# Optimization experiments

Measured on AMD Instinct MI355X. Metric: run time of the kernel, lower is better.

Reference implementation:

```python
import jax, jax.numpy as jnp
import numpy as np

N, E, D_IN, D_HID, D_OUT = 50000, 800000, 128, 128, 64

def setup_inputs() -> dict:
    key = jax.random.key(0)
    ks = jax.random.split(key, 20)
    inp = {
        'x': jax.random.normal(ks[0], (N, D_IN), dtype=jnp.float32),
        'edge_index': jax.random.randint(ks[1], (2, E), 0, N, dtype=jnp.int64),
        'edge_attr': jax.random.normal(ks[2], (E, 16), dtype=jnp.float32),
        'edge_weight': jax.random.uniform(ks[3], (E,), dtype=jnp.float32),
    }
    dims = [(D_IN, D_HID), (D_HID, D_HID), (D_HID, D_OUT)]
    for i, (di, do) in enumerate(dims):
        s = 1.0 / np.sqrt(di)
        inp[f'Wl{i}'] = jax.random.uniform(ks[4 + 5 * i], (di, do), minval=-s, maxval=s, dtype=jnp.float32)
        inp[f'bl{i}'] = jnp.zeros((do,), dtype=jnp.float32)
        inp[f'Wr{i}'] = jax.random.uniform(ks[5 + 5 * i], (di, do), minval=-s, maxval=s, dtype=jnp.float32)
        inp[f'Ws{i}'] = jax.random.uniform(ks[6 + 5 * i], (di, do), minval=-s, maxval=s, dtype=jnp.float32)
        inp[f'bs{i}'] = jnp.zeros((do,), dtype=jnp.float32)
    return inp


def _sage(x, src, dst, Wl, bl, Wr):
    # mean aggregation of source features at target nodes (PyG SAGEConv)
    msg = x[src]                                               # [E, d] gather
    ssum = jax.ops.segment_sum(msg, dst, num_segments=N)        # [N, d]
    cnt = jax.ops.segment_sum(jnp.ones((src.shape[0],), x.dtype), dst, num_segments=N)
    agg = ssum / jnp.maximum(cnt, 1.0)[:, None]
    return agg @ Wl + bl + x @ Wr                               # lin_l(agg) + lin_r(x)


def reference(x, edge_index, edge_attr, edge_weight,
              Wl0, bl0, Wr0, Ws0, bs0,
              Wl1, bl1, Wr1, Ws1, bs1,
              Wl2, bl2, Wr2, Ws2, bs2):
    src, dst = edge_index[0], edge_index[1]
    h = jax.nn.relu(_sage(x, src, dst, Wl0, bl0, Wr0) + x @ Ws0 + bs0)
    h = jax.nn.relu(_sage(h, src, dst, Wl1, bl1, Wr1) + h @ Ws1 + bs1)
    out = _sage(h, src, dst, Wl2, bl2, Wr2) + h @ Ws2 + bs2
    return out
```

## Files before the change

kernel.cpp:

```cpp
#include <hip/hip_runtime.h>
#include <hip/hip_bf16.h>


#define LB __launch_bounds__

typedef __attribute__((ext_vector_type(8))) short short8;
typedef __attribute__((ext_vector_type(4))) float f32x4;

__device__ __forceinline__ unsigned short bf16_rne(float f) {
  unsigned u = __builtin_bit_cast(unsigned, f);
  unsigned r = u + 0x7fffu + ((u >> 16) & 1u);
  return (unsigned short)(r >> 16);
}
__device__ __forceinline__ float bf16_to_f(unsigned short us) {
  return __builtin_bit_cast(float, (unsigned)us << 16);
}
__device__ __forceinline__ float bits_to_f(unsigned u) {
  return __builtin_bit_cast(float, u);
}

__device__ __forceinline__ void async16(const void* g, void* l) {
  __builtin_amdgcn_global_load_lds((const __attribute__((address_space(1))) unsigned*)g,
                                   (__attribute__((address_space(3))) unsigned*)l, 16, 0, 0);
}

#define BCAP 8192
#define P1_CHUNK 4096

__device__ __forceinline__ void p1_body(int bid, const int* __restrict__ src,
                                        const int* __restrict__ dst, int* __restrict__ bcnt,
                                        int2* __restrict__ pairs, int E) {
  __shared__ int cnt[256];
  __shared__ int base[256];
  const int tid = threadIdx.x;
  cnt[tid] = 0;
  __syncthreads();
  const int e0 = bid * P1_CHUNK;
  int myb[16], myr[16], mys[16], myd[16];
#pragma unroll
  for (int i = 0; i < 16; ++i) {
    int e = e0 + i * 256 + tid;
    myb[i] = -1;
    if (e < E) {
      int s = src[e], d = dst[e];
      int b = d >> 8;
      myb[i] = b;
      mys[i] = s;
      myd[i] = d;
      myr[i] = atomicAdd(&cnt[b], 1);
    }
  }
  __syncthreads();
  base[tid] = (cnt[tid] > 0) ? atomicAdd(&bcnt[tid], cnt[tid]) : 0;
  __syncthreads();
#pragma unroll
  for (int i = 0; i < 16; ++i) {
    int b = myb[i];
    if (b >= 0) {
      int p = base[b] + myr[i];
      if (p < BCAP) pairs[(size_t)b * BCAP + p] = make_int2(mys[i], myd[i]);
    }
  }
}

__device__ __forceinline__ void p234_body(int b, const int2* __restrict__ pairs,
                                          const int* __restrict__ bcnt, int* __restrict__ gcounter,
                                          int* __restrict__ row_start, int* __restrict__ deg_arr,
                                          float* __restrict__ scale, int* __restrict__ srcs, int N) {
  __shared__ int h[256];
  __shared__ int sc[256];
  __shared__ int cur[256];
  __shared__ int shared_bb;
  const int tid = threadIdx.x;
  h[tid] = 0;
  __syncthreads();
  int m = bcnt[b];
  if (m > BCAP) m = BCAP;
  for (int i = tid; i < m; i += 256) {
    atomicAdd(&h[pairs[(size_t)b * BCAP + i].y & 255], 1);
  }
  __syncthreads();
  const int deg = h[tid];
  sc[tid] = deg;
  __syncthreads();
  for (int off = 1; off < 256; off <<= 1) {
    int add = (tid >= off) ? sc[tid - off] : 0;
    __syncthreads();
    sc[tid] += add;
    __syncthreads();
  }
  if (tid == 0) shared_bb = atomicAdd(gcounter, sc[255]);
  __syncthreads();
  const int abs_off = shared_bb + sc[tid] - deg;
  const int node = b * 256 + tid;
  if (node < N) {
    row_start[node] = abs_off;
    deg_arr[node] = deg;
    scale[node] = 1.0f / (float)(deg > 1 ? deg : 1);
  }
  cur[tid] = abs_off;
  __syncthreads();
  for (int i = tid; i < m; i += 256) {
    int2 pr = pairs[(size_t)b * BCAP + i];
    int p = atomicAdd(&cur[pr.y & 255], 1);
    srcs[p] = pr.x;
  }
}

__device__ __forceinline__ void wpack_body(int wb, const float* __restrict__ Wl0,
                                           const float* __restrict__ Wr0,
                                           const float* __restrict__ Ws0,
                                           const float* __restrict__ bl0,
                                           const float* __restrict__ bs0,
                                           const float* __restrict__ Wl1,
                                           const float* __restrict__ Wr1,
                                           const float* __restrict__ Ws1,
                                           const float* __restrict__ bl1,
                                           const float* __restrict__ bs1,
                                           const float* __restrict__ Wl2,
                                           const float* __restrict__ Wr2,
                                           const float* __restrict__ Ws2,
                                           const float* __restrict__ bl2,
                                           const float* __restrict__ bs2, ushort* __restrict__ Bh0,
                                           ushort* __restrict__ Bo0, float* __restrict__ bb0,
                                           ushort* __restrict__ Bh1, ushort* __restrict__ Bo1,
                                           float* __restrict__ bb1, ushort* __restrict__ Bh2,
                                           ushort* __restrict__ Bo2, float* __restrict__ bb2) {
  const int layer = wb >> 7;
  const int xb = wb & 127;
  const float *Wl, *Wr, *Ws, *bl, *bs;
  ushort *Bh, *Bo;
  float* bb;
  int M;
  if (layer == 0) {
    Wl = Wl0; Wr = Wr0; Ws = Ws0; bl = bl0; bs = bs0; Bh = Bh0; Bo = Bo0; bb = bb0; M = 256;
  } else if (layer == 1) {
    Wl = Wl1; Wr = Wr1; Ws = Ws1; bl = bl1; bs = bs1; Bh = Bh1; Bo = Bo1; bb = bb1; M = 256;
  } else {
    Wl = Wl2; Wr = Wr2; Ws = Ws2; bl = bl2; bs = bs2; Bh = Bh2; Bo = Bo2; bb = bb2; M = 128;
  }
  const int DO = M / 2;
  int idx = xb * 256 + (int)threadIdx.x;
  if (idx < 128 * M) {
    int k = idx / M, c = idx - k * M;
    float v = (c < DO) ? Wl[k * DO + c] : (Wr[k * DO + (c - DO)] + Ws[k * DO + (c - DO)]);
    unsigned short h = bf16_rne(v);
    unsigned short l = bf16_rne(v - bf16_to_f(h));
    int d = ((k >> 3) * M + c) * 8 + (k & 7);
    Bh[d] = h;
    Bo[d] = l;
  }
  if (idx < DO) bb[idx] = bl[idx] + bs[idx];
}

__device__ __forceinline__ void split8v(f32x4 f0, f32x4 f1, short8& h, short8& l) {
  float f[8] = {f0[0], f0[1], f0[2], f0[3], f1[0], f1[1], f1[2], f1[3]};
#pragma unroll
  for (int j = 0; j < 8; ++j) {
    unsigned u = __builtin_bit_cast(unsigned, f[j]);
    h[j] = (short)(u >> 16);
    l[j] = (short)bf16_rne(f[j] - bits_to_f(u & 0xffff0000u));
  }
}

template <int M, bool AFP32>
__device__ __forceinline__ void gemm_body(int bx, const float* __restrict__ Af,
                                          const ushort* __restrict__ Ahi,
                                          const ushort* __restrict__ Alo,
                                          const ushort* __restrict__ Bhi,
                                          const ushort* __restrict__ Blo, ushort* __restrict__ Yb,
                                          float* __restrict__ Z, int n, char* smem) {
  constexpr int DO = M / 2;
  constexpr int NWC = (M >= 256) ? 4 : 2;
  constexpr int NWR = 4 / NWC;
  constexpr int BROWS = 32 * NWR;
  const int tid = threadIdx.x;
  const int w = tid >> 6, l = tid & 63;
  const int q = l >> 4, m16 = l & 15;
  const int blockRow0 = bx * BROWS;
  const int rowBase = blockRow0 + (w / NWC) * 32;
  const int colBase = (w % NWC) * 64;
  const int wbase = tid & ~63;

  if (AFP32) {
#pragma unroll
    for (int r = 0; r < BROWS / 8; ++r) {
      int ell = r * 256 + tid;
      int row = ell >> 5, gl = ell & 31;
      int grow = blockRow0 + row;
      if (grow >= n) grow = n - 1;
      int gs = gl ^ (row & 15);
      async16(Af + (size_t)grow * 128 + gs * 4, smem + (size_t)(r * 256 + wbase) * 16);
    }
  } else {
#pragma unroll
    for (int r = 0; r < BROWS / 16; ++r) {
      int ell = r * 256 + tid;
      int row = ell >> 4, gl = ell & 15;
      int grow = blockRow0 + row;
      if (grow >= n) grow = n - 1;
      int gs = gl ^ (row & 15);
      async16(Ahi + (size_t)grow * 128 + gs * 8, smem + (size_t)(r * 256 + wbase) * 16);
      async16(Alo + (size_t)grow * 128 + gs * 8,
              smem + (size_t)BROWS * 256 + (size_t)(r * 256 + wbase) * 16);
    }
  }
  __syncthreads();

  f32x4 acc[2][4] = {};
  const int rl0 = (w / NWC) * 32 + m16;

#pragma unroll
  for (int s = 0; s < 4; ++s) {
    short8 ah[2], al[2], bh[4], bo[4];
#pragma unroll
    for (int i = 0; i < 2; ++i) {
      int rl = rl0 + i * 16;
      if (AFP32) {
        int g0 = (2 * (s * 4 + q)) ^ m16;
        int g1 = (2 * (s * 4 + q) + 1) ^ m16;
        f32x4 fa = *(const f32x4*)(smem + (size_t)rl * 512 + g0 * 16);
        f32x4 fb = *(const f32x4*)(smem + (size_t)rl * 512 + g1 * 16);
        split8v(fa, fb, ah[i], al[i]);
      } else {
        int g = (s * 4 + q) ^ m16;
        ah[i] = *(const short8*)(smem + (size_t)rl * 256 + g * 16);
        al[i] = *(const short8*)(smem + (size_t)BROWS * 256 + (size_t)rl * 256 + g * 16);
      }
    }
    const int kb = s * 4 + q;
#pragma unroll
    for (int j = 0; j < 4; ++j) {
      size_t off = ((size_t)kb * M + colBase + j * 16 + m16) * 8;
      bh[j] = *(const short8*)(Bhi + off);
      bo[j] = *(const short8*)(Blo + off);
    }
#pragma unroll
    for (int i = 0; i < 2; ++i)
#pragma unroll
      for (int j = 0; j < 4; ++j) {
        acc[i][j] = __builtin_amdgcn_mfma_f32_16x16x32_bf16(ah[i], bh[j], acc[i][j], 0, 0, 0);
        acc[i][j] = __builtin_amdgcn_mfma_f32_16x16x32_bf16(ah[i], bo[j], acc[i][j], 0, 0, 0);
        acc[i][j] = __builtin_amdgcn_mfma_f32_16x16x32_bf16(al[i], bh[j], acc[i][j], 0, 0, 0);
      }
  }

#pragma unroll
  for (int i = 0; i < 2; ++i) {
    int rb = rowBase + i * 16 + q * 4;
#pragma unroll
    for (int j = 0; j < 4; ++j) {
      int c = colBase + j * 16 + m16;
#pragma unroll
      for (int r = 0; r < 4; ++r) {
        int row = rb + r;
        if (row < n) {
          float v = acc[i][j][r];
          if (c < DO)
            Yb[(size_t)row * DO + c] = bf16_rne(v);
          else
            Z[(size_t)row * DO + (c - DO)] = v;
        }
      }
    }
  }
}

template <int M, bool AFP32>
__global__ LB(256, 3) void mfma_gemm_kernel(const float* __restrict__ Af,
                                            const ushort* __restrict__ Ahi,
                                            const ushort* __restrict__ Alo,
                                            const ushort* __restrict__ Bhi,
                                            const ushort* __restrict__ Blo,
                                            ushort* __restrict__ Yb, float* __restrict__ Z, int n) {
  constexpr int LDSB = AFP32 ? (32 * 512) : ((M >= 256 ? 32 : 64) * 512);
  __shared__ __align__(16) char smem[LDSB];
  gemm_body<M, AFP32>(blockIdx.x, Af, Ahi, Alo, Bhi, Blo, Yb, Z, n, smem);
}

__global__ LB(256) void fused_wpack_p1(const int* __restrict__ src, const int* __restrict__ dst,
                                       int* __restrict__ bcnt, int2* __restrict__ pairs, int E,
                                       int NP1, const float* Wl0, const float* Wr0, const float* Ws0,
                                       const float* bl0, const float* bs0, const float* Wl1,
                                       const float* Wr1, const float* Ws1, const float* bl1,
                                       const float* bs1, const float* Wl2, const float* Wr2,
                                       const float* Ws2, const float* bl2, const float* bs2,
                                       ushort* Bh0, ushort* Bo0, float* bb0, ushort* Bh1,
                                       ushort* Bo1, float* bb1, ushort* Bh2, ushort* Bo2,
                                       float* bb2) {
  if ((int)blockIdx.x < NP1) {
    p1_body(blockIdx.x, src, dst, bcnt, pairs, E);
  } else {
    wpack_body(blockIdx.x - NP1, Wl0, Wr0, Ws0, bl0, bs0, Wl1, Wr1, Ws1, bl1, bs1, Wl2, Wr2, Ws2,
               bl2, bs2, Bh0, Bo0, bb0, Bh1, Bo1, bb1, Bh2, Bo2, bb2);
  }
}

__global__ LB(256, 3) void fused_p234_gemm0(const int2* __restrict__ pairs,
                                            const int* __restrict__ bcnt, int* __restrict__ gcounter,
                                            int* __restrict__ row_start, int* __restrict__ deg_arr,
                                            float* __restrict__ scale, int* __restrict__ srcs, int N,
                                            const float* __restrict__ x,
                                            const ushort* __restrict__ Bh0,
                                            const ushort* __restrict__ Bo0, ushort* __restrict__ Yb,
                                            float* __restrict__ Zf, int NB) {
  __shared__ __align__(16) char smem[32 * 512];
  if ((int)blockIdx.x < NB) {
    p234_body(blockIdx.x, pairs, bcnt, gcounter, row_start, deg_arr, scale, srcs, N);
  } else {
    gemm_body<256, true>(blockIdx.x - NB, x, nullptr, nullptr, Bh0, Bo0, Yb, Zf, N, smem);
  }
}

__global__ LB(256) void agg128_kernel(const ushort* __restrict__ Y, const float* __restrict__ Z,
                                      const int* __restrict__ row_start,
                                      const int* __restrict__ deg_arr, const int* __restrict__ srcs,
                                      const float* __restrict__ scale,
                                      const float* __restrict__ bsum, unsigned* __restrict__ Hhi,
                                      unsigned* __restrict__ Hlo, int n) {
  int node = blockIdx.x * 4 + (threadIdx.x >> 6);
  if (node >= n) return;
  const int lane = threadIdx.x & 63;
  const int li = lane & 31;
  const int half = lane >> 5;
  const int e0 = row_start[node];
  const int cnt = deg_arr[node];
  const int end = e0 + cnt;
  const int c1 = cnt < 64 ? cnt : 64;
  int idx = (lane < c1) ? srcs[e0 + lane] : 0;
  const uint2* Yu = (const uint2*)Y;
  float a0 = 0.f, a1 = 0.f, a2 = 0.f, a3 = 0.f;

  int j = 0;
  for (; j + 16 <= c1; j += 16) {
    int s[8];
#pragma unroll
    for (int t = 0; t < 8; ++t) s[t] = __shfl(idx, j + 2 * t + half);
    uint2 u[8];
#pragma unroll
    for (int t = 0; t < 8; ++t) u[t] = Yu[(size_t)s[t] * 32 + li];
#pragma unroll
    for (int t = 0; t < 8; ++t) {
      a0 += bits_to_f(u[t].x << 16);
      a1 += bits_to_f(u[t].x & 0xffff0000u);
      a2 += bits_to_f(u[t].y << 16);
      a3 += bits_to_f(u[t].y & 0xffff0000u);
    }
  }
  if (j + 8 <= c1) {
    int s[4];
#pragma unroll
    for (int t = 0; t < 4; ++t) s[t] = __shfl(idx, j + 2 * t + half);
    uint2 u[4];
#pragma unroll
    for (int t = 0; t < 4; ++t) u[t] = Yu[(size_t)s[t] * 32 + li];
#pragma unroll
    for (int t = 0; t < 4; ++t) {
      a0 += bits_to_f(u[t].x << 16);
      a1 += bits_to_f(u[t].x & 0xffff0000u);
      a2 += bits_to_f(u[t].y << 16);
      a3 += bits_to_f(u[t].y & 0xffff0000u);
    }
    j += 8;
  }
  for (; j + 2 <= c1; j += 2) {
    int s = __shfl(idx, j + half);
    uint2 u = Yu[(size_t)s * 32 + li];
    a0 += bits_to_f(u.x << 16);
    a1 += bits_to_f(u.x & 0xffff0000u);
    a2 += bits_to_f(u.y << 16);
    a3 += bits_to_f(u.y & 0xffff0000u);
  }
  if (j < c1) {
    int s = __shfl(idx, j);
    if (half == 0) {
      uint2 u = Yu[(size_t)s * 32 + li];
      a0 += bits_to_f(u.x << 16);
      a1 += bits_to_f(u.x & 0xffff0000u);
      a2 += bits_to_f(u.y << 16);
      a3 += bits_to_f(u.y & 0xffff0000u);
    }
  }
  if (cnt > 64) {
    int e = e0 + 64;
    for (; e + 2 <= end; e += 2) {
      int s = srcs[e + half];
      uint2 u = Yu[(size_t)s * 32 + li];
      a0 += bits_to_f(u.x << 16);
      a1 += bits_to_f(u.x & 0xffff0000u);
      a2 += bits_to_f(u.y << 16);
      a3 += bits_to_f(u.y & 0xffff0000u);
    }
    if (e < end && half == 0) {
      int s = srcs[e];
      uint2 u = Yu[(size_t)s * 32 + li];
      a0 += bits_to_f(u.x << 16);
      a1 += bits_to_f(u.x & 0xffff0000u);
      a2 += bits_to_f(u.y << 16);
      a3 += bits_to_f(u.y & 0xffff0000u);
    }
  }
  a0 += __shfl(a0, lane ^ 32);
  a1 += __shfl(a1, lane ^ 32);
  a2 += __shfl(a2, lane ^ 32);
  a3 += __shfl(a3, lane ^ 32);

  float sc = scale[node];
  float4 z = ((const float4*)Z)[(size_t)node * 32 + li];
  float4 b = ((const float4*)bsum)[li];
  float o0 = fmaxf(z.x + sc * a0 + b.x, 0.f);
  float o1 = fmaxf(z.y + sc * a1 + b.y, 0.f);
  float o2 = fmaxf(z.z + sc * a2 + b.z, 0.f);
  float o3 = fmaxf(z.w + sc * a3 + b.w, 0.f);
  unsigned short h0 = bf16_rne(o0), h1 = bf16_rne(o1), h2 = bf16_rne(o2), h3 = bf16_rne(o3);
  if (half == 0) {
    uint2 hp;
    hp.x = (unsigned)h0 | ((unsigned)h1 << 16);
    hp.y = (unsigned)h2 | ((unsigned)h3 << 16);
    ((uint2*)Hhi)[(size_t)node * 32 + li] = hp;
  } else {
    unsigned short l0 = bf16_rne(o0 - bf16_to_f(h0));
    unsigned short l1 = bf16_rne(o1 - bf16_to_f(h1));
    unsigned short l2 = bf16_rne(o2 - bf16_to_f(h2));
    unsigned short l3 = bf16_rne(o3 - bf16_to_f(h3));
    uint2 lp;
    lp.x = (unsigned)l0 | ((unsigned)l1 << 16);
    lp.y = (unsigned)l2 | ((unsigned)l3 << 16);
    ((uint2*)Hlo)[(size_t)node * 32 + li] = lp;
  }
}

__global__ LB(256) void agg64_kernel(const ushort* __restrict__ Y, const float* __restrict__ Z,
                                     const int* __restrict__ row_start,
                                     const int* __restrict__ deg_arr, const int* __restrict__ srcs,
                                     const float* __restrict__ scale, const float* __restrict__ bsum,
                                     float* __restrict__ out, int n) {
  int node = blockIdx.x * 4 + (threadIdx.x >> 6);
  if (node >= n) return;
  const int lane = threadIdx.x & 63;
  const int li = lane & 15;
  const int qt = lane >> 4;
  const int e0 = row_start[node];
  const int cnt = deg_arr[node];
  const int end = e0 + cnt;
  const int c1 = cnt < 64 ? cnt : 64;
  int idx = (lane < c1) ? srcs[e0 + lane] : 0;
  const uint2* Yu = (const uint2*)Y;
  float a0 = 0.f, a1 = 0.f, a2 = 0.f, a3 = 0.f;

  int j = 0;
  for (; j + 16 <= c1; j += 16) {
    int s0 = __shfl(idx, j + qt);
    int s1 = __shfl(idx, j + 4 + qt);
    int s2 = __shfl(idx, j + 8 + qt);
    int s3 = __shfl(idx, j + 12 + qt);
    uint2 u0 = Yu[(size_t)s0 * 16 + li];
    uint2 u1 = Yu[(size_t)s1 * 16 + li];
    uint2 u2 = Yu[(size_t)s2 * 16 + li];
    uint2 u3 = Yu[(size_t)s3 * 16 + li];
    a0 += bits_to_f(u0.x << 16) + bits_to_f(u1.x << 16) + bits_to_f(u2.x << 16) +
          bits_to_f(u3.x << 16);
    a1 += bits_to_f(u0.x & 0xffff0000u) + bits_to_f(u1.x & 0xffff0000u) +
          bits_to_f(u2.x & 0xffff0000u) + bits_to_f(u3.x & 0xffff0000u);
    a2 += bits_to_f(u0.y << 16) + bits_to_f(u1.y << 16) + bits_to_f(u2.y << 16) +
          bits_to_f(u3.y << 16);
    a3 += bits_to_f(u0.y & 0xffff0000u) + bits_to_f(u1.y & 0xffff0000u) +
          bits_to_f(u2.y & 0xffff0000u) + bits_to_f(u3.y & 0xffff0000u);
  }
  for (; j + 4 <= c1; j += 4) {
    int s = __shfl(idx, j + qt);
    uint2 u = Yu[(size_t)s * 16 + li];
    a0 += bits_to_f(u.x << 16);
    a1 += bits_to_f(u.x & 0xffff0000u);
    a2 += bits_to_f(u.y << 16);
    a3 += bits_to_f(u.y & 0xffff0000u);
  }
  {
    int rem = c1 - j;
    if (rem > 0) {
      int s = __shfl(idx, j + (qt < rem ? qt : 0));
      if (qt < rem) {
        uint2 u = Yu[(size_t)s * 16 + li];
        a0 += bits_to_f(u.x << 16);
        a1 += bits_to_f(u.x & 0xffff0000u);
        a2 += bits_to_f(u.y << 16);
        a3 += bits_to_f(u.y & 0xffff0000u);
      }
    }
  }
  if (cnt > 64) {
    int e = e0 + 64;
    for (; e + 4 <= end; e += 4) {
      int s = srcs[e + qt];
      uint2 u = Yu[(size_t)s * 16 + li];
      a0 += bits_to_f(u.x << 16);
      a1 += bits_to_f(u.x & 0xffff0000u);
      a2 += bits_to_f(u.y << 16);
      a3 += bits_to_f(u.y & 0xffff0000u);
    }
    int rem = end - e;
    if (qt < rem) {
      int s = srcs[e + qt];
      uint2 u = Yu[(size_t)s * 16 + li];
      a0 += bits_to_f(u.x << 16);
      a1 += bits_to_f(u.x & 0xffff0000u);
      a2 += bits_to_f(u.y << 16);
      a3 += bits_to_f(u.y & 0xffff0000u);
    }
  }
  a0 += __shfl(a0, lane ^ 16);
  a1 += __shfl(a1, lane ^ 16);
  a2 += __shfl(a2, lane ^ 16);
  a3 += __shfl(a3, lane ^ 16);
  a0 += __shfl(a0, lane ^ 32);
  a1 += __shfl(a1, lane ^ 32);
  a2 += __shfl(a2, lane ^ 32);
  a3 += __shfl(a3, lane ^ 32);

  if (qt == 0) {
    float sc = scale[node];
    float4 z = ((const float4*)Z)[(size_t)node * 16 + li];
    float4 b = ((const float4*)bsum)[li];
    float4 o;
    o.x = z.x + sc * a0 + b.x;
    o.y = z.y + sc * a1 + b.y;
    o.z = z.z + sc * a2 + b.z;
    o.w = z.w + sc * a3 + b.w;
    ((float4*)out)[(size_t)node * 16 + li] = o;
  }
}

extern "C" void kernel_launch(void* const* d_in, const int* in_sizes, int n_in,
                              void* d_out, int out_size, void* d_ws, size_t ws_size,
                              hipStream_t stream) {
  const float* x = (const float*)d_in[0];
  const int* ei = (const int*)d_in[1];
  const int N = in_sizes[0] / 128;
  const int E = in_sizes[3];
  const int* src = ei;
  const int* dst = ei + E;
  const float* Wl[3] = {(const float*)d_in[4], (const float*)d_in[9], (const float*)d_in[14]};
  const float* bl[3] = {(const float*)d_in[5], (const float*)d_in[10], (const float*)d_in[15]};
  const float* Wr[3] = {(const float*)d_in[6], (const float*)d_in[11], (const float*)d_in[16]};
  const float* Ws[3] = {(const float*)d_in[7], (const float*)d_in[12], (const float*)d_in[17]};
  const float* bs[3] = {(const float*)d_in[8], (const float*)d_in[13], (const float*)d_in[18]};

  const int NB = (N + 255) >> 8;
  const int NP1 = (E + P1_CHUNK - 1) / P1_CHUNK;

  size_t off = 0;
  auto carve = [&](size_t bytes) -> char* {
    char* p = (char*)d_ws + off;
    off += (bytes + 255) & ~(size_t)255;
    return p;
  };
  int* row_start = (int*)carve((size_t)N * 4);
  int* deg_arr = (int*)carve((size_t)N * 4);
  int* bcnt = (int*)carve((size_t)NB * 4);
  int* gcounter = (int*)carve(256);
  float* scale = (float*)carve((size_t)N * 4);
  int* srcs = (int*)carve((size_t)E * 4);
  int2* pairs = (int2*)carve((size_t)NB * BCAP * 8);
  ushort* Hhi = (ushort*)carve((size_t)N * 128 * 2);
  ushort* Hlo = (ushort*)carve((size_t)N * 128 * 2);
  ushort* Yb = (ushort*)carve((size_t)N * 128 * 2);
  float* Zf = (float*)carve((size_t)N * 128 * 4);
  ushort* Bh[3];
  ushort* Bo[3];
  float* bsum[3];
  for (int i = 0; i < 3; ++i) {
    Bh[i] = (ushort*)carve(128 * 256 * 2);
    Bo[i] = (ushort*)carve(128 * 256 * 2);
    bsum[i] = (float*)carve(128 * 4);
  }
  (void)ws_size;
  (void)n_in;
  (void)out_size;

  size_t bcnt_pad = ((size_t)NB * 4 + 255) & ~(size_t)255;
  hipMemsetAsync(bcnt, 0, bcnt_pad + 4, stream);

  fused_wpack_p1<<<NP1 + 384, 256, 0, stream>>>(
      src, dst, bcnt, pairs, E, NP1, Wl[0], Wr[0], Ws[0], bl[0], bs[0], Wl[1], Wr[1], Ws[1], bl[1],
      bs[1], Wl[2], Wr[2], Ws[2], bl[2], bs[2], Bh[0], Bo[0], bsum[0], Bh[1], Bo[1], bsum[1], Bh[2],
      Bo[2], bsum[2]);

  int g32 = (N + 31) / 32;
  int g64 = (N + 63) / 64;
  int gAgg = (N + 3) / 4;

  fused_p234_gemm0<<<NB + g32, 256, 0, stream>>>(pairs, bcnt, gcounter, row_start, deg_arr, scale,
                                                 srcs, N, x, Bh[0], Bo[0], Yb, Zf, NB);
  agg128_kernel<<<gAgg, 256, 0, stream>>>(Yb, Zf, row_start, deg_arr, srcs, scale, bsum[0],
                                          (unsigned*)Hhi, (unsigned*)Hlo, N);
  mfma_gemm_kernel<256, false><<<g32, 256, 0, stream>>>(nullptr, Hhi, Hlo, Bh[1], Bo[1], Yb, Zf, N);
  agg128_kernel<<<gAgg, 256, 0, stream>>>(Yb, Zf, row_start, deg_arr, srcs, scale, bsum[1],
                                          (unsigned*)Hhi, (unsigned*)Hlo, N);
  mfma_gemm_kernel<128, false><<<g64, 256, 0, stream>>>(nullptr, Hhi, Hlo, Bh[2], Bo[2], Yb, Zf, N);
  agg64_kernel<<<gAgg, 256, 0, stream>>>(Yb, Zf, row_start, deg_arr, srcs, scale, bsum[2],
                                         (float*)d_out, N);
}
```

Baseline: 301.9 us.

## Fuse mean-aggregation into following layer's MFMA GEMM via LDS staging

```diff
diff --git a/kernel.cpp b/kernel.cpp
--- a/kernel.cpp
+++ b/kernel.cpp
@@ -163,13 +163,12 @@
   }
 }
 
-template <int M, bool AFP32>
-__device__ __forceinline__ void gemm_body(int bx, const float* __restrict__ Af,
-                                          const ushort* __restrict__ Ahi,
-                                          const ushort* __restrict__ Alo,
-                                          const ushort* __restrict__ Bhi,
-                                          const ushort* __restrict__ Blo, ushort* __restrict__ Yb,
-                                          float* __restrict__ Z, int n, char* smem) {
+template <int M>
+__device__ __forceinline__ void gemm_compute(int bx, const char* smem,
+                                             const ushort* __restrict__ Bhi,
+                                             const ushort* __restrict__ Blo,
+                                             ushort* __restrict__ Yb, float* __restrict__ Z,
+                                             int n) {
   constexpr int DO = M / 2;
   constexpr int NWC = (M >= 256) ? 4 : 2;
   constexpr int NWR = 4 / NWC;
@@ -177,35 +176,8 @@
   const int tid = threadIdx.x;
   const int w = tid >> 6, l = tid & 63;
   const int q = l >> 4, m16 = l & 15;
-  const int blockRow0 = bx * BROWS;
-  const int rowBase = blockRow0 + (w / NWC) * 32;
+  const int rowBase = bx * BROWS + (w / NWC) * 32;
   const int colBase = (w % NWC) * 64;
-  const int wbase = tid & ~63;
-
-  if (AFP32) {
-#pragma unroll
-    for (int r = 0; r < BROWS / 8; ++r) {
-      int ell = r * 256 + tid;
-      int row = ell >> 5, gl = ell & 31;
-      int grow = blockRow0 + row;
-      if (grow >= n) grow = n - 1;
-      int gs = gl ^ (row & 15);
-      async16(Af + (size_t)grow * 128 + gs * 4, smem + (size_t)(r * 256 + wbase) * 16);
-    }
-  } else {
-#pragma unroll
-    for (int r = 0; r < BROWS / 16; ++r) {
-      int ell = r * 256 + tid;
-      int row = ell >> 4, gl = ell & 15;
-      int grow = blockRow0 + row;
-      if (grow >= n) grow = n - 1;
-      int gs = gl ^ (row & 15);
-      async16(Ahi + (size_t)grow * 128 + gs * 8, smem + (size_t)(r * 256 + wbase) * 16);
-      async16(Alo + (size_t)grow * 128 + gs * 8,
-              smem + (size_t)BROWS * 256 + (size_t)(r * 256 + wbase) * 16);
-    }
-  }
-  __syncthreads();
 
   f32x4 acc[2][4] = {};
   const int rl0 = (w / NWC) * 32 + m16;
@@ -213,22 +185,16 @@
 #pragma unroll
   for (int s = 0; s < 4; ++s) {
     short8 ah[2], al[2], bh[4], bo[4];
+    const int kb = s * 4 + q;
 #pragma unroll
     for (int i = 0; i < 2; ++i) {
       int rl = rl0 + i * 16;
-      if (AFP32) {
-        int g0 = (2 * (s * 4 + q)) ^ m16;
-        int g1 = (2 * (s * 4 + q) + 1) ^ m16;
-        f32x4 fa = *(const f32x4*)(smem + (size_t)rl * 512 + g0 * 16);
-        f32x4 fb = *(const f32x4*)(smem + (size_t)rl * 512 + g1 * 16);
-        split8v(fa, fb, ah[i], al[i]);
-      } else {
-        int g = (s * 4 + q) ^ m16;
-        ah[i] = *(const short8*)(smem + (size_t)rl * 256 + g * 16);
-        al[i] = *(const short8*)(smem + (size_t)BROWS * 256 + (size_t)rl * 256 + g * 16);
-      }
-    }
-    const int kb = s * 4 + q;
+      int g0 = (2 * kb) ^ m16;
+      int g1 = (2 * kb + 1) ^ m16;
+      f32x4 fa = *(const f32x4*)(smem + (size_t)rl * 512 + g0 * 16);
+      f32x4 fb = *(const f32x4*)(smem + (size_t)rl * 512 + g1 * 16);
+      split8v(fa, fb, ah[i], al[i]);
+    }
 #pragma unroll
     for (int j = 0; j < 4; ++j) {
       size_t off = ((size_t)kb * M + colBase + j * 16 + m16) * 8;
@@ -266,16 +232,153 @@
   }
 }
 
-template <int M, bool AFP32>
-__global__ LB(256, 3) void mfma_gemm_kernel(const float* __restrict__ Af,
-                                            const ushort* __restrict__ Ahi,
-                                            const ushort* __restrict__ Alo,
-                                            const ushort* __restrict__ Bhi,
-                                            const ushort* __restrict__ Blo,
-                                            ushort* __restrict__ Yb, float* __restrict__ Z, int n) {
-  constexpr int LDSB = AFP32 ? (32 * 512) : ((M >= 256 ? 32 : 64) * 512);
-  __shared__ __align__(16) char smem[LDSB];
-  gemm_body<M, AFP32>(blockIdx.x, Af, Ahi, Alo, Bhi, Blo, Yb, Z, n, smem);
+__device__ __forceinline__ void gemm0_body(int bx, const float* __restrict__ x,
+                                           const ushort* __restrict__ Bh,
+                                           const ushort* __restrict__ Bo, ushort* __restrict__ Yb,
+                                           float* __restrict__ Z, int n, char* smem) {
+  const int tid = threadIdx.x;
+  const int wbase = tid & ~63;
+#pragma unroll
+  for (int r = 0; r < 4; ++r) {
+    int ell = r * 256 + tid;
+    int row = ell >> 5, gl = ell & 31;
+    int grow = bx * 32 + row;
+    if (grow >= n) grow = n - 1;
+    int gs = gl ^ (row & 15);
+    async16(x + (size_t)grow * 128 + gs * 4, smem + (size_t)(r * 256 + wbase) * 16);
+  }
+  __syncthreads();
+  gemm_compute<256>(bx, smem, Bh, Bo, Yb, Z, n);
+}
+
+__device__ __forceinline__ void agg_gather128(const uint2* __restrict__ Yu,
+                                              const int* __restrict__ srcs, int e0, int cnt,
+                                              int lane, int li, int half, float& a0, float& a1,
+                                              float& a2, float& a3) {
+  const int end = e0 + cnt;
+  const int c1 = cnt < 64 ? cnt : 64;
+  int idx = (lane < c1) ? srcs[e0 + lane] : 0;
+  int j = 0;
+  for (; j + 16 <= c1; j += 16) {
+    int s[8];
+#pragma unroll
+    for (int t = 0; t < 8; ++t) s[t] = __shfl(idx, j + 2 * t + half);
+    uint2 u[8];
+#pragma unroll
+    for (int t = 0; t < 8; ++t) u[t] = Yu[(size_t)s[t] * 32 + li];
+#pragma unroll
+    for (int t = 0; t < 8; ++t) {
+      a0 += bits_to_f(u[t].x << 16);
+      a1 += bits_to_f(u[t].x & 0xffff0000u);
+      a2 += bits_to_f(u[t].y << 16);
+      a3 += bits_to_f(u[t].y & 0xffff0000u);
+    }
+  }
+  if (j + 8 <= c1) {
+    int s[4];
+#pragma unroll
+    for (int t = 0; t < 4; ++t) s[t] = __shfl(idx, j + 2 * t + half);
+    uint2 u[4];
+#pragma unroll
+    for (int t = 0; t < 4; ++t) u[t] = Yu[(size_t)s[t] * 32 + li];
+#pragma unroll
+    for (int t = 0; t < 4; ++t) {
+      a0 += bits_to_f(u[t].x << 16);
+      a1 += bits_to_f(u[t].x & 0xffff0000u);
+      a2 += bits_to_f(u[t].y << 16);
+      a3 += bits_to_f(u[t].y & 0xffff0000u);
+    }
+    j += 8;
+  }
+  for (; j + 2 <= c1; j += 2) {
+    int s = __shfl(idx, j + half);
+    uint2 u = Yu[(size_t)s * 32 + li];
+    a0 += bits_to_f(u.x << 16);
+    a1 += bits_to_f(u.x & 0xffff0000u);
+    a2 += bits_to_f(u.y << 16);
+    a3 += bits_to_f(u.y & 0xffff0000u);
+  }
+  if (j < c1) {
+    int s = __shfl(idx, j);
+    if (half == 0) {
+      uint2 u = Yu[(size_t)s * 32 + li];
+      a0 += bits_to_f(u.x << 16);
+      a1 += bits_to_f(u.x & 0xffff0000u);
+      a2 += bits_to_f(u.y << 16);
+      a3 += bits_to_f(u.y & 0xffff0000u);
+    }
+  }
+  if (cnt > 64) {
+    int e = e0 + 64;
+    for (; e + 2 <= end; e += 2) {
+      int s = srcs[e + half];
+      uint2 u = Yu[(size_t)s * 32 + li];
+      a0 += bits_to_f(u.x << 16);
+      a1 += bits_to_f(u.x & 0xffff0000u);
+      a2 += bits_to_f(u.y << 16);
+      a3 += bits_to_f(u.y & 0xffff0000u);
+    }
+    if (e < end && half == 0) {
+      int s = srcs[e];
+      uint2 u = Yu[(size_t)s * 32 + li];
+      a0 += bits_to_f(u.x << 16);
+      a1 += bits_to_f(u.x & 0xffff0000u);
+      a2 += bits_to_f(u.y << 16);
+      a3 += bits_to_f(u.y & 0xffff0000u);
+    }
+  }
+}
+
+template <int M>
+__global__ LB(256, 3) void fused_agg_gemm(const ushort* __restrict__ Y,
+                                          const float* __restrict__ Zprev,
+                                          const int* __restrict__ row_start,
+                                          const int* __restrict__ deg_arr,
+                                          const int* __restrict__ srcs,
+                                          const float* __restrict__ scale,
+                                          const float* __restrict__ bsum,
+                                          const ushort* __restrict__ Bhi,
+                                          const ushort* __restrict__ Blo, ushort* __restrict__ Yb,
+                                          float* __restrict__ Zf, int n) {
+  constexpr int BROWS = (M >= 256) ? 32 : 64;
+  __shared__ __align__(16) char smem[BROWS * 512];
+  const int tid = threadIdx.x;
+  const int w = tid >> 6;
+  const int lane = tid & 63;
+  const int li = lane & 31;
+  const int half = lane >> 5;
+  const int blockRow0 = blockIdx.x * BROWS;
+  const uint2* Yu = (const uint2*)Y;
+
+#pragma unroll 1
+  for (int t = 0; t < BROWS / 4; ++t) {
+    const int r = t * 4 + w;
+    const int node = blockRow0 + r;
+    float a0 = 0.f, a1 = 0.f, a2 = 0.f, a3 = 0.f;
+    const bool live = node < n;
+    if (live) {
+      agg_gather128(Yu, srcs, row_start[node], deg_arr[node], lane, li, half, a0, a1, a2, a3);
+    }
+    a0 += __shfl(a0, lane ^ 32);
+    a1 += __shfl(a1, lane ^ 32);
+    a2 += __shfl(a2, lane ^ 32);
+    a3 += __shfl(a3, lane ^ 32);
+    float4 o = make_float4(0.f, 0.f, 0.f, 0.f);
+    if (live) {
+      float sc = scale[node];
+      float4 z = ((const float4*)Zprev)[(size_t)node * 32 + li];
+      float4 b = ((const float4*)bsum)[li];
+      o.x = fmaxf(z.x + sc * a0 + b.x, 0.f);
+      o.y = fmaxf(z.y + sc * a1 + b.y, 0.f);
+      o.z = fmaxf(z.z + sc * a2 + b.z, 0.f);
+      o.w = fmaxf(z.w + sc * a3 + b.w, 0.f);
+    }
+    if (half == 0) {
+      *(float4*)(smem + (size_t)r * 512 + (size_t)((li ^ (r & 15)) * 16)) = o;
+    }
+  }
+  __syncthreads();
+  gemm_compute<M>(blockIdx.x, smem, Bhi, Blo, Yb, Zf, n);
 }
 
 __global__ LB(256) void fused_wpack_p1(const int* __restrict__ src, const int* __restrict__ dst,
@@ -308,125 +411,7 @@
   if ((int)blockIdx.x < NB) {
     p234_body(blockIdx.x, pairs, bcnt, gcounter, row_start, deg_arr, scale, srcs, N);
   } else {
-    gemm_body<256, true>(blockIdx.x - NB, x, nullptr, nullptr, Bh0, Bo0, Yb, Zf, N, smem);
-  }
-}
-
-__global__ LB(256) void agg128_kernel(const ushort* __restrict__ Y, const float* __restrict__ Z,
-                                      const int* __restrict__ row_start,
-                                      const int* __restrict__ deg_arr, const int* __restrict__ srcs,
-                                      const float* __restrict__ scale,
-                                      const float* __restrict__ bsum, unsigned* __restrict__ Hhi,
-                                      unsigned* __restrict__ Hlo, int n) {
-  int node = blockIdx.x * 4 + (threadIdx.x >> 6);
-  if (node >= n) return;
-  const int lane = threadIdx.x & 63;
-  const int li = lane & 31;
-  const int half = lane >> 5;
-  const int e0 = row_start[node];
-  const int cnt = deg_arr[node];
-  const int end = e0 + cnt;
-  const int c1 = cnt < 64 ? cnt : 64;
-  int idx = (lane < c1) ? srcs[e0 + lane] : 0;
-  const uint2* Yu = (const uint2*)Y;
-  float a0 = 0.f, a1 = 0.f, a2 = 0.f, a3 = 0.f;
-
-  int j = 0;
-  for (; j + 16 <= c1; j += 16) {
-    int s[8];
-#pragma unroll
-    for (int t = 0; t < 8; ++t) s[t] = __shfl(idx, j + 2 * t + half);
-    uint2 u[8];
-#pragma unroll
-    for (int t = 0; t < 8; ++t) u[t] = Yu[(size_t)s[t] * 32 + li];
-#pragma unroll
-    for (int t = 0; t < 8; ++t) {
-      a0 += bits_to_f(u[t].x << 16);
-      a1 += bits_to_f(u[t].x & 0xffff0000u);
-      a2 += bits_to_f(u[t].y << 16);
-      a3 += bits_to_f(u[t].y & 0xffff0000u);
-    }
-  }
-  if (j + 8 <= c1) {
-    int s[4];
-#pragma unroll
-    for (int t = 0; t < 4; ++t) s[t] = __shfl(idx, j + 2 * t + half);
-    uint2 u[4];
-#pragma unroll
-    for (int t = 0; t < 4; ++t) u[t] = Yu[(size_t)s[t] * 32 + li];
-#pragma unroll
-    for (int t = 0; t < 4; ++t) {
-      a0 += bits_to_f(u[t].x << 16);
-      a1 += bits_to_f(u[t].x & 0xffff0000u);
-      a2 += bits_to_f(u[t].y << 16);
-      a3 += bits_to_f(u[t].y & 0xffff0000u);
-    }
-    j += 8;
-  }
-  for (; j + 2 <= c1; j += 2) {
-    int s = __shfl(idx, j + half);
-    uint2 u = Yu[(size_t)s * 32 + li];
-    a0 += bits_to_f(u.x << 16);
-    a1 += bits_to_f(u.x & 0xffff0000u);
-    a2 += bits_to_f(u.y << 16);
-    a3 += bits_to_f(u.y & 0xffff0000u);
-  }
-  if (j < c1) {
-    int s = __shfl(idx, j);
-    if (half == 0) {
-      uint2 u = Yu[(size_t)s * 32 + li];
-      a0 += bits_to_f(u.x << 16);
-      a1 += bits_to_f(u.x & 0xffff0000u);
-      a2 += bits_to_f(u.y << 16);
-      a3 += bits_to_f(u.y & 0xffff0000u);
-    }
-  }
-  if (cnt > 64) {
-    int e = e0 + 64;
-    for (; e + 2 <= end; e += 2) {
-      int s = srcs[e + half];
-      uint2 u = Yu[(size_t)s * 32 + li];
-      a0 += bits_to_f(u.x << 16);
-      a1 += bits_to_f(u.x & 0xffff0000u);
-      a2 += bits_to_f(u.y << 16);
-      a3 += bits_to_f(u.y & 0xffff0000u);
-    }
-    if (e < end && half == 0) {
-      int s = srcs[e];
-      uint2 u = Yu[(size_t)s * 32 + li];
-      a0 += bits_to_f(u.x << 16);
-      a1 += bits_to_f(u.x & 0xffff0000u);
-      a2 += bits_to_f(u.y << 16);
-      a3 += bits_to_f(u.y & 0xffff0000u);
-    }
-  }
-  a0 += __shfl(a0, lane ^ 32);
-  a1 += __shfl(a1, lane ^ 32);
-  a2 += __shfl(a2, lane ^ 32);
-  a3 += __shfl(a3, lane ^ 32);
-
-  float sc = scale[node];
-  float4 z = ((const float4*)Z)[(size_t)node * 32 + li];
-  float4 b = ((const float4*)bsum)[li];
-  float o0 = fmaxf(z.x + sc * a0 + b.x, 0.f);
-  float o1 = fmaxf(z.y + sc * a1 + b.y, 0.f);
-  float o2 = fmaxf(z.z + sc * a2 + b.z, 0.f);
-  float o3 = fmaxf(z.w + sc * a3 + b.w, 0.f);
-  unsigned short h0 = bf16_rne(o0), h1 = bf16_rne(o1), h2 = bf16_rne(o2), h3 = bf16_rne(o3);
-  if (half == 0) {
-    uint2 hp;
-    hp.x = (unsigned)h0 | ((unsigned)h1 << 16);
-    hp.y = (unsigned)h2 | ((unsigned)h3 << 16);
-    ((uint2*)Hhi)[(size_t)node * 32 + li] = hp;
-  } else {
-    unsigned short l0 = bf16_rne(o0 - bf16_to_f(h0));
-    unsigned short l1 = bf16_rne(o1 - bf16_to_f(h1));
-    unsigned short l2 = bf16_rne(o2 - bf16_to_f(h2));
-    unsigned short l3 = bf16_rne(o3 - bf16_to_f(h3));
-    uint2 lp;
-    lp.x = (unsigned)l0 | ((unsigned)l1 << 16);
-    lp.y = (unsigned)l2 | ((unsigned)l3 << 16);
-    ((uint2*)Hlo)[(size_t)node * 32 + li] = lp;
+    gemm0_body(blockIdx.x - NB, x, Bh0, Bo0, Yb, Zf, N, smem);
   }
 }
 
@@ -561,10 +546,10 @@
   float* scale = (float*)carve((size_t)N * 4);
   int* srcs = (int*)carve((size_t)E * 4);
   int2* pairs = (int2*)carve((size_t)NB * BCAP * 8);
-  ushort* Hhi = (ushort*)carve((size_t)N * 128 * 2);
-  ushort* Hlo = (ushort*)carve((size_t)N * 128 * 2);
-  ushort* Yb = (ushort*)carve((size_t)N * 128 * 2);
-  float* Zf = (float*)carve((size_t)N * 128 * 4);
+  ushort* Yb0 = (ushort*)carve((size_t)N * 128 * 2);
+  float* Zf0 = (float*)carve((size_t)N * 128 * 4);
+  ushort* Yb1 = (ushort*)carve((size_t)N * 128 * 2);
+  float* Zf1 = (float*)carve((size_t)N * 128 * 4);
   ushort* Bh[3];
   ushort* Bo[3];
   float* bsum[3];
@@ -590,13 +575,11 @@
   int gAgg = (N + 3) / 4;
 
   fused_p234_gemm0<<<NB + g32, 256, 0, stream>>>(pairs, bcnt, gcounter, row_start, deg_arr, scale,
-                                                 srcs, N, x, Bh[0], Bo[0], Yb, Zf, NB);
-  agg128_kernel<<<gAgg, 256, 0, stream>>>(Yb, Zf, row_start, deg_arr, srcs, scale, bsum[0],
-                                          (unsigned*)Hhi, (unsigned*)Hlo, N);
-  mfma_gemm_kernel<256, false><<<g32, 256, 0, stream>>>(nullptr, Hhi, Hlo, Bh[1], Bo[1], Yb, Zf, N);
-  agg128_kernel<<<gAgg, 256, 0, stream>>>(Yb, Zf, row_start, deg_arr, srcs, scale, bsum[1],
-                                          (unsigned*)Hhi, (unsigned*)Hlo, N);
-  mfma_gemm_kernel<128, false><<<g64, 256, 0, stream>>>(nullptr, Hhi, Hlo, Bh[2], Bo[2], Yb, Zf, N);
-  agg64_kernel<<<gAgg, 256, 0, stream>>>(Yb, Zf, row_start, deg_arr, srcs, scale, bsum[2],
+                                                 srcs, N, x, Bh[0], Bo[0], Yb0, Zf0, NB);
+  fused_agg_gemm<256><<<g32, 256, 0, stream>>>(Yb0, Zf0, row_start, deg_arr, srcs, scale, bsum[0],
+                                               Bh[1], Bo[1], Yb1, Zf1, N);
+  fused_agg_gemm<128><<<g64, 256, 0, stream>>>(Yb1, Zf1, row_start, deg_arr, srcs, scale, bsum[1],
+                                               Bh[2], Bo[2], Yb0, Zf0, N);
+  agg64_kernel<<<gAgg, 256, 0, stream>>>(Yb0, Zf0, row_start, deg_arr, srcs, scale, bsum[2],
                                          (float*)d_out, N);
 }
```

New measurement: 306.7 us. About the same (+1.6%).
